# Kernel tuning notes

Hardware: AMD Instinct MI355X
Metric: run time of the kernel (lower is better)

The kernel has to match this reference:

```python
import jax, jax.numpy as jnp
import numpy as np

D = 1024      # d_model
H = 16        # num_heads
K = D // H    # head_dim = 64
S = 3         # num_scales
R = 2         # compression_ratio
ROPE_BASE = 10000.0


def _rope(x, pos, inv_freq):
    # x: [B, N, H, K]; pos: [N] float positions (already scaled per scale)
    ang = pos[:, None] * inv_freq[None, :]              # [N, K//2]
    cos = jnp.cos(ang)[None, :, None, :]                # [1, N, 1, K//2]
    sin = jnp.sin(ang)[None, :, None, :]
    x1, x2 = jnp.split(x, 2, axis=-1)
    return jnp.concatenate([x1 * cos - x2 * sin, x1 * sin + x2 * cos], axis=-1)


def _scale_attn(x, v, Wq_l, bq_l, Wk_l, bk_l, inv_freq, scale_idx):
    # x, v: [B, N, D]
    B, N, Dm = x.shape
    q = (x @ Wq_l.T + bq_l).reshape(B, N, H, K)
    k = (x @ Wk_l.T + bk_l).reshape(B, N, H, K)
    vh = v.reshape(B, N, H, K)
    # per-scale adjusted positions: stride compression_ratio**scale_idx
    pos = jnp.arange(N, dtype=jnp.float32) * jnp.float32(R ** scale_idx)
    q = _rope(q, pos, inv_freq)
    k = _rope(k, pos, inv_freq)
    scale = 1.0 / jnp.sqrt(jnp.float32(K))
    scores = jnp.einsum('bqhk,bmhk->bhqm', q, k) * scale   # [B, H, N, N]
    causal = jnp.triu(jnp.ones((N, N), dtype=bool), k=1)
    scores = jnp.where(causal[None, None], jnp.finfo(scores.dtype).min, scores)
    w = jax.nn.softmax(scores, axis=-1)
    ctx = jnp.einsum('bhqm,bmhk->bqhk', w, vh).reshape(B, N, Dm)
    return ctx


def setup_inputs() -> dict:
    key = jax.random.key(0)
    ks = jax.random.split(key, 11)
    B, N = 1, 2048
    lim = 1.0 / np.sqrt(D)  # eqx.nn.Linear default uniform init bound
    u = lambda k, shp: jax.random.uniform(k, shp, jnp.float32, -lim, lim)
    return {
        'x0': jax.random.normal(ks[0], (B, N, D), jnp.float32),
        'x1': jax.random.normal(ks[1], (B, N // R, D), jnp.float32),
        'x2': jax.random.normal(ks[2], (B, N // R ** 2, D), jnp.float32),
        'Wq': u(ks[3], (S, D, D)),
        'bq': u(ks[4], (S, D)),
        'Wk': u(ks[5], (S, D, D)),
        'bk': u(ks[6], (S, D)),
        'Wv': u(ks[7], (D, D)),
        'bv': u(ks[8], (D,)),
        'Wo': u(ks[9], (D, D)),
        'bo': u(ks[10], (D,)),
    }


def reference(x0, x1, x2, Wq, bq, Wk, bk, Wv, bv, Wo, bo):
    inv_freq = 1.0 / (ROPE_BASE ** (jnp.arange(0, K, 2, dtype=jnp.float32) / K))
    # shared V: computed once at scale 0, decomposed (avg-pooled) per scale
    v_base = x0 @ Wv.T + bv                               # [B, N, D]
    B, N0, Dm = v_base.shape
    outs = []
    for i, x in enumerate((x0, x1, x2)):
        if i == 0:
            v = v_base
        else:
            p = R ** i
            v = v_base.reshape(B, N0 // p, p, Dm).mean(axis=2)
        ctx = _scale_attn(x, v, Wq[i], bq[i], Wk[i], bk[i], inv_freq, i)
        outs.append(ctx @ Wo.T + bo)
    return tuple(outs)
```

## Files before the change

kernel.cpp:

```cpp
#include <hip/hip_runtime.h>
#include <hip/hip_bf16.h>
#include <math.h>

typedef __bf16 bf16x8 __attribute__((ext_vector_type(8)));
typedef __bf16 bf16x4 __attribute__((ext_vector_type(4)));
typedef __bf16 bf16x2 __attribute__((ext_vector_type(2)));
typedef float f32x4 __attribute__((ext_vector_type(4)));
typedef float f32x16 __attribute__((ext_vector_type(16)));

static constexpr int DM = 1024;
static constexpr int HD = 64;
static constexpr size_t M1 = 1024 * 1024;

__device__ __forceinline__ unsigned pk2(float a, float b) {
    union { __bf16 h[2]; unsigned u; } t;
    t.h[0] = (__bf16)a; t.h[1] = (__bf16)b;
    return t.u;
}

typedef const __attribute__((address_space(1))) unsigned int* gp_t;
typedef __attribute__((address_space(3))) unsigned int* lp_t;
__device__ __forceinline__ void gload_lds16(const void* g, void* l) {
    __builtin_amdgcn_global_load_lds((gp_t)g, (lp_t)l, 16, 0, 0);
}

__global__ void cvt_all(const float* __restrict__ x0, const float* __restrict__ x1,
                        const float* __restrict__ x2, const float* __restrict__ Wq,
                        const float* __restrict__ Wk, const float* __restrict__ Wv,
                        const float* __restrict__ Wo,
                        __bf16* __restrict__ xb0, __bf16* __restrict__ xb1,
                        __bf16* __restrict__ xb2, __bf16* __restrict__ Wqb,
                        __bf16* __restrict__ Wkb, __bf16* __restrict__ Wvb,
                        __bf16* __restrict__ Wob) {
    size_t i = (size_t)(blockIdx.x * blockDim.x + threadIdx.x) * 8;
    const float* in; __bf16* outp; size_t off;
    if      (i < 2 * M1)            { in = x0; outp = xb0; off = i; }
    else if (i < 3 * M1)            { in = x1; outp = xb1; off = i - 2 * M1; }
    else if (i < 3 * M1 + M1 / 2)   { in = x2; outp = xb2; off = i - 3 * M1; }
    else if (i < 6 * M1 + M1 / 2)   { in = Wq; outp = Wqb; off = i - (3 * M1 + M1 / 2); }
    else if (i < 9 * M1 + M1 / 2)   { in = Wk; outp = Wkb; off = i - (6 * M1 + M1 / 2); }
    else if (i < 10 * M1 + M1 / 2)  { in = Wv; outp = Wvb; off = i - (9 * M1 + M1 / 2); }
    else if (i < 11 * M1 + M1 / 2)  { in = Wo; outp = Wob; off = i - (10 * M1 + M1 / 2); }
    else return;
    const float4 a = *reinterpret_cast<const float4*>(in + off);
    const float4 b = *reinterpret_cast<const float4*>(in + off + 4);
    bf16x8 r;
    r[0] = (__bf16)a.x; r[1] = (__bf16)a.y; r[2] = (__bf16)a.z; r[3] = (__bf16)a.w;
    r[4] = (__bf16)b.x; r[5] = (__bf16)b.y; r[6] = (__bf16)b.z; r[7] = (__bf16)b.w;
    *reinterpret_cast<bf16x8*>(outp + off) = r;
}

__device__ __forceinline__ void gemm_lds_core(const __bf16* __restrict__ A,
                                              const __bf16* __restrict__ W,
                                              int rb, int cb, int tix,
                                              __bf16* lA, __bf16* lB,
                                              f32x4 (&acc)[4][4]) {
    const int lane = tix & 63;
    const int w = tix >> 6;
    const int g = lane >> 4, t = lane & 15;
    const int r0 = tix >> 2;
    const int r1 = r0 + 64;
    const int c0 = (tix & 3) ^ ((r0 ^ (r0 >> 2)) & 3);
    const int c1 = (tix & 3) ^ ((r1 ^ (r1 >> 2)) & 3);
    const __bf16* a0 = A + (size_t)(rb + r0) * DM + c0 * 8;
    const __bf16* a1 = A + (size_t)(rb + r1) * DM + c1 * 8;
    const __bf16* b0 = W + (size_t)(cb + r0) * DM + c0 * 8;
    const __bf16* b1 = W + (size_t)(cb + r1) * DM + c1 * 8;
    const int d0 = w * 512;
    const int d1 = 2048 + w * 512;
    const int rw = (w >> 1) * 64, cw = (w & 1) * 64;
    int roA[4], roB[4];
#pragma unroll
    for (int i = 0; i < 4; ++i) {
        const int ra = rw + i * 16 + t;
        const int rbr = cw + i * 16 + t;
        roA[i] = ra * 32 + ((g ^ ((ra ^ (ra >> 2)) & 3)) * 8);
        roB[i] = rbr * 32 + ((g ^ ((rbr ^ (rbr >> 2)) & 3)) * 8);
    }

    gload_lds16(a0, lA + d0);
    gload_lds16(a1, lA + d1);
    gload_lds16(b0, lB + d0);
    gload_lds16(b1, lB + d1);
    __syncthreads();

    int cur = 0;
    for (int kk = 0; kk < DM; kk += 32) {
        if (kk + 32 < DM) {
            __bf16* nA = lA + (cur ^ 1) * 4096;
            __bf16* nB = lB + (cur ^ 1) * 4096;
            gload_lds16(a0 + kk + 32, nA + d0);
            gload_lds16(a1 + kk + 32, nA + d1);
            gload_lds16(b0 + kk + 32, nB + d0);
            gload_lds16(b1 + kk + 32, nB + d1);
        }
        const __bf16* bA = lA + cur * 4096;
        const __bf16* bB = lB + cur * 4096;
        bf16x8 af[4], bfr[4];
#pragma unroll
        for (int i = 0; i < 4; ++i) {
            af[i]  = *reinterpret_cast<const bf16x8*>(bA + roA[i]);
            bfr[i] = *reinterpret_cast<const bf16x8*>(bB + roB[i]);
        }
#pragma unroll
        for (int mi = 0; mi < 4; ++mi)
#pragma unroll
            for (int ni = 0; ni < 4; ++ni)
                acc[mi][ni] = __builtin_amdgcn_mfma_f32_16x16x32_bf16(af[mi], bfr[ni], acc[mi][ni], 0, 0, 0);
        __syncthreads();
        cur ^= 1;
    }
}

__global__ __launch_bounds__(256)
void gemm_pre(const __bf16* __restrict__ xb0, const __bf16* __restrict__ xb1,
              const __bf16* __restrict__ xb2, const __bf16* __restrict__ Wqb,
              const __bf16* __restrict__ Wkb, const __bf16* __restrict__ Wvb,
              const float* __restrict__ bq, const float* __restrict__ bk,
              const float* __restrict__ bv,
              __bf16* __restrict__ qb0, __bf16* __restrict__ kb0,
              __bf16* __restrict__ qb1, __bf16* __restrict__ kb1,
              __bf16* __restrict__ qb2, __bf16* __restrict__ kb2,
              __bf16* __restrict__ vt0, __bf16* __restrict__ vt1,
              __bf16* __restrict__ vt2) {
    __shared__ __align__(16) __bf16 lA[8192], lB[8192];
    const int bid = blockIdx.x;
    const int swz = (bid & 7) * 72 + (bid >> 3);
    int z, local, mblk;
    if      (swz < 128) { z = 0; local = swz;       mblk = 16; }
    else if (swz < 256) { z = 1; local = swz - 128; mblk = 16; }
    else if (swz < 320) { z = 2; local = swz - 256; mblk = 8;  }
    else if (swz < 384) { z = 3; local = swz - 320; mblk = 8;  }
    else if (swz < 416) { z = 4; local = swz - 384; mblk = 4;  }
    else if (swz < 448) { z = 5; local = swz - 416; mblk = 4;  }
    else                { z = 6; local = swz - 448; mblk = 16; }
    const __bf16* A; const __bf16* W; const float* bias; __bf16* out;
    switch (z) {
        case 0:  A = xb0; W = Wqb;          bias = bq;        out = qb0; break;
        case 1:  A = xb0; W = Wkb;          bias = bk;        out = kb0; break;
        case 2:  A = xb1; W = Wqb + M1;     bias = bq + 1024; out = qb1; break;
        case 3:  A = xb1; W = Wkb + M1;     bias = bk + 1024; out = kb1; break;
        case 4:  A = xb2; W = Wqb + 2 * M1; bias = bq + 2048; out = qb2; break;
        case 5:  A = xb2; W = Wkb + 2 * M1; bias = bk + 2048; out = kb2; break;
        default: A = xb0; W = Wvb;          bias = bv;        out = nullptr; break;
    }
    const int rb = (local % mblk) * 128;
    const int cb = (local / mblk) * 128;
    const int tix = threadIdx.x;
    f32x4 acc[4][4] = {};
    gemm_lds_core(A, W, rb, cb, tix, lA, lB, acc);

    const int lane = tix & 63;
    const int w = tix >> 6;
    const int g = lane >> 4, t = lane & 15;
    const int rbw = rb + (w >> 1) * 64;
    const int cbw = cb + (w & 1) * 64;

    if (z == 6) {
#pragma unroll
        for (int ni = 0; ni < 4; ++ni) {
            const int col = cbw + ni * 16 + t;
            const float bb = bias[col];
#pragma unroll
            for (int mi = 0; mi < 4; ++mi) {
                const int row0 = rbw + mi * 16 + g * 4;
                const f32x4 a = acc[mi][ni];
                bf16x4 pk;
#pragma unroll
                for (int r = 0; r < 4; ++r) pk[r] = (__bf16)(a[r] + bb);
                *reinterpret_cast<bf16x4*>(vt0 + (size_t)col * 2048 + row0) = pk;
                bf16x2 p2;
                p2[0] = (__bf16)(0.5f * (a[0] + a[1]) + bb);
                p2[1] = (__bf16)(0.5f * (a[2] + a[3]) + bb);
                *reinterpret_cast<bf16x2*>(vt1 + (size_t)col * 1024 + row0 / 2) = p2;
                vt2[(size_t)col * 512 + row0 / 4] =
                    (__bf16)(0.25f * (a[0] + a[1] + a[2] + a[3]) + bb);
            }
        }
    } else {
        const float qmul = (z & 1) ? 1.0f : 0.125f;
        const float ps = (float)(1 << (z >> 1));
#pragma unroll
        for (int ni = 0; ni < 2; ++ni) {
            const int j = ni * 16 + t;
            const float invf = __expf(-(float)j * 0.28782313662425576f);
            const float b1 = bias[cbw + j];
            const float b2 = bias[cbw + j + 32];
#pragma unroll
            for (int mi = 0; mi < 4; ++mi) {
#pragma unroll
                for (int r = 0; r < 4; ++r) {
                    const int row = rbw + mi * 16 + g * 4 + r;
                    float c, s;
                    __sincosf((float)row * ps * invf, &s, &c);
                    const float x1 = acc[mi][ni][r] + b1;
                    const float x2 = acc[mi][ni + 2][r] + b2;
                    out[(size_t)row * DM + cbw + j]      = (__bf16)((x1 * c - x2 * s) * qmul);
                    out[(size_t)row * DM + cbw + j + 32] = (__bf16)((x1 * s + x2 * c) * qmul);
                }
            }
        }
    }
}

__global__ __launch_bounds__(256)
void attn_all(const __bf16* __restrict__ qb0, const __bf16* __restrict__ kb0,
              const __bf16* __restrict__ vt0, __bf16* __restrict__ ctx0,
              const __bf16* __restrict__ qb1, const __bf16* __restrict__ kb1,
              const __bf16* __restrict__ vt1, __bf16* __restrict__ ctx1,
              const __bf16* __restrict__ qb2, const __bf16* __restrict__ kb2,
              const __bf16* __restrict__ vt2, __bf16* __restrict__ ctx2) {
    __shared__ __align__(16) float shm[4 * 64 * 33];
    const int bid = blockIdx.x;
    const int job = (bid & 7) * 224 + (bid >> 3);
    const int h = job / 112;
    int rem = job % 112;
    const __bf16 *qb, *kb, *vt; __bf16* ctx; int N, nq;
    if (rem < 64)      { qb = qb0; kb = kb0; vt = vt0; ctx = ctx0; N = 2048; nq = 64; }
    else if (rem < 96) { rem -= 64; qb = qb1; kb = kb1; vt = vt1; ctx = ctx1; N = 1024; nq = 32; }
    else               { rem -= 96; qb = qb2; kb = kb2; vt = vt2; ctx = ctx2; N = 512;  nq = 16; }
    const int qt = (rem & 1) ? (nq - 1 - (rem >> 1)) : (rem >> 1);
    const int lane = threadIdx.x & 63;
    const int w = threadIdx.x >> 6;
    const int q0 = qt * 32;
    const int lq = lane & 31;
    const int hi = lane >> 5;

    __bf16* Kl = (__bf16*)shm + (size_t)w * 4096;
    __bf16* Vl = Kl + 2048;

    const __bf16* qp = qb + (size_t)(q0 + lq) * DM + h * HD + hi * 8;
    bf16x8 qf[4];
#pragma unroll
    for (int dc = 0; dc < 4; ++dc)
        qf[dc] = *reinterpret_cast<const bf16x8*>(qp + dc * 16);

    f32x16 o0 = {}, o1 = {};
    float lsum = 0.f;
    const int ktiles = qt + 1;

    const int krow = lane >> 3, kch = lane & 7;
    const int vrow = lane >> 2, vch = lane & 3;

    int koff[4];
#pragma unroll
    for (int dc = 0; dc < 4; ++dc)
        koff[dc] = lq * 64 + (((dc * 2 + hi) ^ (lq & 7)) * 8);
    const int v00o = lq * 32 + ((hi ^ (lq & 3)) * 8);
    const int v01o = lq * 32 + (((2 + hi) ^ (lq & 3)) * 8);
    const int v10o = (32 + lq) * 32 + ((hi ^ (lq & 3)) * 8);
    const int v11o = (32 + lq) * 32 + (((2 + hi) ^ (lq & 3)) * 8);

    unsigned* pw = (unsigned*)Kl + lq * 18;
    const __bf16* prb = (const __bf16*)pw;

    for (int kt = w; kt < ktiles; kt += 4) {
        const int j0 = kt * 32;
#pragma unroll
        for (int j = 0; j < 4; ++j) {
            const int row = j * 8 + krow;
            gload_lds16(kb + (size_t)(j0 + row) * DM + h * HD + ((kch ^ (row & 7)) * 8),
                        Kl + j * 512);
        }
#pragma unroll
        for (int j = 0; j < 4; ++j) {
            const int row = j * 16 + vrow;
            gload_lds16(vt + (size_t)(h * HD + row) * N + j0 + ((vch ^ (row & 3)) * 8),
                        Vl + j * 512);
        }
        asm volatile("s_waitcnt vmcnt(4)" ::: "memory");

        bf16x8 kf[4];
#pragma unroll
        for (int dc = 0; dc < 4; ++dc)
            kf[dc] = *reinterpret_cast<const bf16x8*>(Kl + koff[dc]);

        f32x16 p = {};
        __builtin_amdgcn_s_setprio(1);
        p = __builtin_amdgcn_mfma_f32_32x32x16_bf16(kf[0], qf[0], p, 0, 0, 0);
        p = __builtin_amdgcn_mfma_f32_32x32x16_bf16(kf[1], qf[1], p, 0, 0, 0);
        p = __builtin_amdgcn_mfma_f32_32x32x16_bf16(kf[2], qf[2], p, 0, 0, 0);
        p = __builtin_amdgcn_mfma_f32_32x32x16_bf16(kf[3], qf[3], p, 0, 0, 0);
        __builtin_amdgcn_s_setprio(0);

#pragma unroll
        for (int r = 0; r < 16; ++r) {
            const int key = j0 + (r & 3) + 8 * (r >> 2) + 4 * hi;
            p[r] = (key <= q0 + lq) ? __expf(p[r]) : 0.f;
            lsum += p[r];
        }

        pw[2 * hi]      = pk2(p[0],  p[1]);
        pw[2 * hi + 1]  = pk2(p[2],  p[3]);
        pw[4 + 2 * hi]  = pk2(p[4],  p[5]);
        pw[5 + 2 * hi]  = pk2(p[6],  p[7]);
        pw[8 + 2 * hi]  = pk2(p[8],  p[9]);
        pw[9 + 2 * hi]  = pk2(p[10], p[11]);
        pw[12 + 2 * hi] = pk2(p[12], p[13]);
        pw[13 + 2 * hi] = pk2(p[14], p[15]);
        union U8 { bf16x4 half[2]; bf16x8 v; };
        U8 pf0, pf1;
        pf0.half[0] = *reinterpret_cast<const bf16x4*>(prb + hi * 8);
        pf0.half[1] = *reinterpret_cast<const bf16x4*>(prb + hi * 8 + 4);
        pf1.half[0] = *reinterpret_cast<const bf16x4*>(prb + 16 + hi * 8);
        pf1.half[1] = *reinterpret_cast<const bf16x4*>(prb + 16 + hi * 8 + 4);

        asm volatile("s_waitcnt vmcnt(0)" ::: "memory");
        const bf16x8 v00 = *reinterpret_cast<const bf16x8*>(Vl + v00o);
        const bf16x8 v01 = *reinterpret_cast<const bf16x8*>(Vl + v01o);
        const bf16x8 v10 = *reinterpret_cast<const bf16x8*>(Vl + v10o);
        const bf16x8 v11 = *reinterpret_cast<const bf16x8*>(Vl + v11o);

        __builtin_amdgcn_s_setprio(1);
        o0 = __builtin_amdgcn_mfma_f32_32x32x16_bf16(v00, pf0.v, o0, 0, 0, 0);
        o0 = __builtin_amdgcn_mfma_f32_32x32x16_bf16(v01, pf1.v, o0, 0, 0, 0);
        o1 = __builtin_amdgcn_mfma_f32_32x32x16_bf16(v10, pf0.v, o1, 0, 0, 0);
        o1 = __builtin_amdgcn_mfma_f32_32x32x16_bf16(v11, pf1.v, o1, 0, 0, 0);
        __builtin_amdgcn_s_setprio(0);
    }

    __syncthreads();
    float* cmb = shm;
    float* my = cmb + ((size_t)w * 64 + lane) * 33;
#pragma unroll
    for (int i = 0; i < 16; ++i) { my[i] = o0[i]; my[16 + i] = o1[i]; }
    my[32] = lsum;
    __syncthreads();
    float tot[8] = {};
    float lt = 0.f;
#pragma unroll
    for (int w2 = 0; w2 < 4; ++w2) {
        const float* src = cmb + ((size_t)w2 * 64 + lane) * 33;
#pragma unroll
        for (int j = 0; j < 8; ++j) tot[j] += src[8 * w + j];
        lt += src[32];
    }
    lt += __shfl_xor(lt, 32);
    const float inv = 1.0f / lt;
    const int dbase = 32 * (w >> 1) + 16 * (w & 1) + 4 * hi;
    __bf16* cp = ctx + (size_t)(q0 + lq) * DM + h * HD;
    bf16x4 s0, s1;
#pragma unroll
    for (int j = 0; j < 4; ++j) {
        s0[j] = (__bf16)(tot[j] * inv);
        s1[j] = (__bf16)(tot[4 + j] * inv);
    }
    *reinterpret_cast<bf16x4*>(cp + dbase) = s0;
    *reinterpret_cast<bf16x4*>(cp + dbase + 8) = s1;
}

__global__ __launch_bounds__(256)
void gemm_out_all(const __bf16* __restrict__ c0, const __bf16* __restrict__ c1,
                  const __bf16* __restrict__ c2, const __bf16* __restrict__ Wob,
                  const float* __restrict__ bo, float* __restrict__ out) {
    __shared__ __align__(16) __bf16 lA[8192], lB[8192];
    const int bid = blockIdx.x;
    const int swz = (bid & 7) * 28 + (bid >> 3);
    int z, local, mblk;
    if      (swz < 128) { z = 0; local = swz;       mblk = 16; }
    else if (swz < 192) { z = 1; local = swz - 128; mblk = 8;  }
    else                { z = 2; local = swz - 192; mblk = 4;  }
    const __bf16* A; float* o;
    switch (z) {
        case 0:  A = c0; o = out;             break;
        case 1:  A = c1; o = out + 2048 * DM; break;
        default: A = c2; o = out + 3072 * DM; break;
    }
    const int rb = (local % mblk) * 128;
    const int cb = (local / mblk) * 128;
    const int tix = threadIdx.x;
    f32x4 acc[4][4] = {};
    gemm_lds_core(A, Wob, rb, cb, tix, lA, lB, acc);

    const int lane = tix & 63;
    const int w = tix >> 6;
    const int g = lane >> 4, t = lane & 15;
    const int rbw = rb + (w >> 1) * 64;
    const int cbw = cb + (w & 1) * 64;
#pragma unroll
    for (int ni = 0; ni < 4; ++ni) {
        const int col = cbw + ni * 16 + t;
        const float bb = bo[col];
#pragma unroll
        for (int mi = 0; mi < 4; ++mi) {
            const int row0 = rbw + mi * 16 + g * 4;
#pragma unroll
            for (int r = 0; r < 4; ++r)
                o[(size_t)(row0 + r) * DM + col] = acc[mi][ni][r] + bb;
        }
    }
}

extern "C" void kernel_launch(void* const* d_in, const int* in_sizes, int n_in,
                              void* d_out, int out_size, void* d_ws, size_t ws_size,
                              hipStream_t stream) {
    const float* x0 = (const float*)d_in[0];
    const float* x1 = (const float*)d_in[1];
    const float* x2 = (const float*)d_in[2];
    const float* Wq = (const float*)d_in[3];
    const float* bq = (const float*)d_in[4];
    const float* Wk = (const float*)d_in[5];
    const float* bk = (const float*)d_in[6];
    const float* Wv = (const float*)d_in[7];
    const float* bv = (const float*)d_in[8];
    const float* Wo = (const float*)d_in[9];
    const float* bo = (const float*)d_in[10];
    float* out = (float*)d_out;

    __bf16* xb0 = (__bf16*)d_ws;
    __bf16* xb1 = xb0 + 2 * M1;
    __bf16* xb2 = xb1 + M1;
    __bf16* Wqb = xb2 + M1 / 2;
    __bf16* Wkb = Wqb + 3 * M1;
    __bf16* Wvb = Wkb + 3 * M1;
    __bf16* Wob = Wvb + M1;
    __bf16* vt0 = Wob + M1;
    __bf16* vt1 = vt0 + 2 * M1;
    __bf16* vt2 = vt1 + M1;
    __bf16* qb0 = vt2 + M1 / 2;
    __bf16* kb0 = qb0 + 2 * M1;
    __bf16* qb1 = kb0 + 2 * M1;
    __bf16* kb1 = qb1 + M1;
    __bf16* qb2 = kb1 + M1;
    __bf16* kb2 = qb2 + M1 / 2;

    cvt_all<<<5888, 256, 0, stream>>>(x0, x1, x2, Wq, Wk, Wv, Wo,
                                      xb0, xb1, xb2, Wqb, Wkb, Wvb, Wob);
    gemm_pre<<<576, 256, 0, stream>>>(xb0, xb1, xb2, Wqb, Wkb, Wvb,
                                      bq, bk, bv,
                                      qb0, kb0, qb1, kb1, qb2, kb2,
                                      vt0, vt1, vt2);
    attn_all<<<1792, 256, 0, stream>>>(qb0, kb0, vt0, qb0,
                                       qb1, kb1, vt1, qb1,
                                       qb2, kb2, vt2, qb2);
    gemm_out_all<<<224, 256, 0, stream>>>(qb0, qb1, qb2, Wob, bo, out);
}
```

Baseline: 140.3 us.

## Split GEMM K dimension across two wave groups per block with LDS reduction

Both projection GEMM kernels now launch 512 threads per block. Each half of the block computes the same 128x128 output tile over half of the K dimension (512 each), using its own LDS buffers. The second half then writes its accumulators to LDS and the first half adds them before the epilogue. The intent is to raise the wave count per tile and shorten each block's serial K loop, given that the grids (576 and 224 blocks) are small relative to the CU count. The cost is 64KB of LDS per block and an extra LDS reduction pass, which may limit occupancy.

Measured after the change: 124.7 us. 11.2% less time.

```diff
diff --git a/kernel.cpp b/kernel.cpp
--- a/kernel.cpp
+++ b/kernel.cpp
@@ -50,18 +50,18 @@
     *reinterpret_cast<bf16x8*>(outp + off) = r;
 }
 
-__device__ __forceinline__ void gemm_lds_core(const __bf16* __restrict__ A,
-                                              const __bf16* __restrict__ W,
-                                              int rb, int cb, int tix,
-                                              __bf16* lA, __bf16* lB,
-                                              f32x4 (&acc)[4][4]) {
-    const int lane = tix & 63;
-    const int w = tix >> 6;
+__device__ __forceinline__ void gemm_lds_core_g(const __bf16* __restrict__ A,
+                                                const __bf16* __restrict__ W,
+                                                int rb, int cb, int ltix,
+                                                __bf16* lA, __bf16* lB,
+                                                f32x4 (&acc)[4][4]) {
+    const int lane = ltix & 63;
+    const int w = ltix >> 6;
     const int g = lane >> 4, t = lane & 15;
-    const int r0 = tix >> 2;
+    const int r0 = ltix >> 2;
     const int r1 = r0 + 64;
-    const int c0 = (tix & 3) ^ ((r0 ^ (r0 >> 2)) & 3);
-    const int c1 = (tix & 3) ^ ((r1 ^ (r1 >> 2)) & 3);
+    const int c0 = (ltix & 3) ^ ((r0 ^ (r0 >> 2)) & 3);
+    const int c1 = (ltix & 3) ^ ((r1 ^ (r1 >> 2)) & 3);
     const __bf16* a0 = A + (size_t)(rb + r0) * DM + c0 * 8;
     const __bf16* a1 = A + (size_t)(rb + r1) * DM + c1 * 8;
     const __bf16* b0 = W + (size_t)(cb + r0) * DM + c0 * 8;
@@ -85,8 +85,8 @@
     __syncthreads();
 
     int cur = 0;
-    for (int kk = 0; kk < DM; kk += 32) {
-        if (kk + 32 < DM) {
+    for (int kk = 0; kk < 512; kk += 32) {
+        if (kk + 32 < 512) {
             __bf16* nA = lA + (cur ^ 1) * 4096;
             __bf16* nB = lB + (cur ^ 1) * 4096;
             gload_lds16(a0 + kk + 32, nA + d0);
@@ -112,7 +112,27 @@
     }
 }
 
-__global__ __launch_bounds__(256)
+__device__ __forceinline__ void spillAcc(float* cmbF, int wq, int lane,
+                                         const f32x4 (&acc)[4][4]) {
+#pragma unroll
+    for (int i = 0; i < 16; ++i) {
+        const f32x4 v = acc[i >> 2][i & 3];
+#pragma unroll
+        for (int r = 0; r < 4; ++r)
+            cmbF[(size_t)(i * 4 + r) * 256 + wq * 64 + lane] = v[r];
+    }
+}
+__device__ __forceinline__ void addAcc(const float* cmbF, int wq, int lane,
+                                       f32x4 (&acc)[4][4]) {
+#pragma unroll
+    for (int i = 0; i < 16; ++i) {
+#pragma unroll
+        for (int r = 0; r < 4; ++r)
+            acc[i >> 2][i & 3][r] += cmbF[(size_t)(i * 4 + r) * 256 + wq * 64 + lane];
+    }
+}
+
+__global__ __launch_bounds__(512)
 void gemm_pre(const __bf16* __restrict__ xb0, const __bf16* __restrict__ xb1,
               const __bf16* __restrict__ xb2, const __bf16* __restrict__ Wqb,
               const __bf16* __restrict__ Wkb, const __bf16* __restrict__ Wvb,
@@ -123,7 +143,7 @@
               __bf16* __restrict__ qb2, __bf16* __restrict__ kb2,
               __bf16* __restrict__ vt0, __bf16* __restrict__ vt1,
               __bf16* __restrict__ vt2) {
-    __shared__ __align__(16) __bf16 lA[8192], lB[8192];
+    __shared__ __align__(16) __bf16 lsh[32768];
     const int bid = blockIdx.x;
     const int swz = (bid & 7) * 72 + (bid >> 3);
     int z, local, mblk;
@@ -147,14 +167,24 @@
     const int rb = (local % mblk) * 128;
     const int cb = (local / mblk) * 128;
     const int tix = threadIdx.x;
+    const int grp = tix >> 8;
+    const int ltix = tix & 255;
+    __bf16* lA = lsh + grp * 8192;
+    __bf16* lB = lsh + 16384 + grp * 8192;
     f32x4 acc[4][4] = {};
-    gemm_lds_core(A, W, rb, cb, tix, lA, lB, acc);
-
-    const int lane = tix & 63;
-    const int w = tix >> 6;
+    gemm_lds_core_g(A + grp * 512, W + grp * 512, rb, cb, ltix, lA, lB, acc);
+
+    float* cmbF = (float*)lsh;
+    const int lane = ltix & 63;
+    const int wq = ltix >> 6;
+    if (grp == 1) spillAcc(cmbF, wq, lane, acc);
+    __syncthreads();
+    if (grp == 1) return;
+    addAcc(cmbF, wq, lane, acc);
+
     const int g = lane >> 4, t = lane & 15;
-    const int rbw = rb + (w >> 1) * 64;
-    const int cbw = cb + (w & 1) * 64;
+    const int rbw = rb + (wq >> 1) * 64;
+    const int cbw = cb + (wq & 1) * 64;
 
     if (z == 6) {
 #pragma unroll
@@ -349,11 +379,11 @@
     *reinterpret_cast<bf16x4*>(cp + dbase + 8) = s1;
 }
 
-__global__ __launch_bounds__(256)
+__global__ __launch_bounds__(512)
 void gemm_out_all(const __bf16* __restrict__ c0, const __bf16* __restrict__ c1,
                   const __bf16* __restrict__ c2, const __bf16* __restrict__ Wob,
                   const float* __restrict__ bo, float* __restrict__ out) {
-    __shared__ __align__(16) __bf16 lA[8192], lB[8192];
+    __shared__ __align__(16) __bf16 lsh[32768];
     const int bid = blockIdx.x;
     const int swz = (bid & 7) * 28 + (bid >> 3);
     int z, local, mblk;
@@ -369,14 +399,24 @@
     const int rb = (local % mblk) * 128;
     const int cb = (local / mblk) * 128;
     const int tix = threadIdx.x;
+    const int grp = tix >> 8;
+    const int ltix = tix & 255;
+    __bf16* lA = lsh + grp * 8192;
+    __bf16* lB = lsh + 16384 + grp * 8192;
     f32x4 acc[4][4] = {};
-    gemm_lds_core(A, Wob, rb, cb, tix, lA, lB, acc);
-
-    const int lane = tix & 63;
-    const int w = tix >> 6;
+    gemm_lds_core_g(A + grp * 512, Wob + grp * 512, rb, cb, ltix, lA, lB, acc);
+
+    float* cmbF = (float*)lsh;
+    const int lane = ltix & 63;
+    const int wq = ltix >> 6;
+    if (grp == 1) spillAcc(cmbF, wq, lane, acc);
+    __syncthreads();
+    if (grp == 1) return;
+    addAcc(cmbF, wq, lane, acc);
+
     const int g = lane >> 4, t = lane & 15;
-    const int rbw = rb + (w >> 1) * 64;
-    const int cbw = cb + (w & 1) * 64;
+    const int rbw = rb + (wq >> 1) * 64;
+    const int cbw = cb + (wq & 1) * 64;
 #pragma unroll
     for (int ni = 0; ni < 4; ++ni) {
         const int col = cbw + ni * 16 + t;
@@ -426,12 +466,12 @@
 
     cvt_all<<<5888, 256, 0, stream>>>(x0, x1, x2, Wq, Wk, Wv, Wo,
                                       xb0, xb1, xb2, Wqb, Wkb, Wvb, Wob);
-    gemm_pre<<<576, 256, 0, stream>>>(xb0, xb1, xb2, Wqb, Wkb, Wvb,
+    gemm_pre<<<576, 512, 0, stream>>>(xb0, xb1, xb2, Wqb, Wkb, Wvb,
                                       bq, bk, bv,
                                       qb0, kb0, qb1, kb1, qb2, kb2,
                                       vt0, vt1, vt2);
     attn_all<<<1792, 256, 0, stream>>>(qb0, kb0, vt0, qb0,
                                        qb1, kb1, vt1, qb1,
                                        qb2, kb2, vt2, qb2);
-    gemm_out_all<<<224, 256, 0, stream>>>(qb0, qb1, qb2, Wob, bo, out);
-}
+    gemm_out_all<<<224, 512, 0, stream>>>(qb0, qb1, qb2, Wob, bo, out);
+}
```
